# Kernel optimization log

Hardware: AMD Instinct MI355X
Metric: run time of the kernel (lower is better)

Reference implementation:

```python
import jax, jax.numpy as jnp
import numpy as np

N_NODES = 50000
N_EDGES = 800000
IN_CH = 256
HID = 64
HEADS = 4
NEG_SLOPE = 0.2  # PyG GATConv default


def setup_inputs() -> dict:
    key = jax.random.key(0)
    ks = jax.random.split(key, 12)
    glorot = lambda k, shape: jax.random.normal(k, shape, jnp.float32) * (2.0 / (shape[0] + shape[-1])) ** 0.5
    d1 = HEADS * HID  # 256: width after conv1 (concat heads)
    return {
        "x": jax.random.normal(ks[0], (N_NODES, IN_CH), jnp.float32),
        "edge_index": jax.random.randint(ks[1], (2, N_EDGES), 0, N_NODES, jnp.int64),
        # conv1: GATConv(IN_CH, HID, heads=HEADS)
        "W1": glorot(ks[2], (IN_CH, HEADS * HID)),
        "a_src1": glorot(ks[3], (HEADS, HID)),
        "a_dst1": glorot(ks[4], (HEADS, HID)),
        "b1": jnp.zeros((HEADS * HID,), jnp.float32),
        # conv2: GATConv(d1, d1, heads=1)
        "W2": glorot(ks[5], (d1, d1)),
        "a_src2": glorot(ks[6], (1, d1)),
        "a_dst2": glorot(ks[7], (1, d1)),
        "b2": jnp.zeros((d1,), jnp.float32),
    }


def gat_conv(x, src, dst, W, a_src, a_dst, b, heads, out_ch, n_nodes):
    """PyG-style GATConv: per-head linear, additive attention, segment softmax over dst."""
    h = (x @ W).reshape(n_nodes, heads, out_ch)            # [N, H, C]
    alpha_src = jnp.sum(h * a_src, axis=-1)                # [N, H]
    alpha_dst = jnp.sum(h * a_dst, axis=-1)                # [N, H]
    e = jax.nn.leaky_relu(alpha_src[src] + alpha_dst[dst], NEG_SLOPE)  # [E, H]
    # numerically-stable segment softmax grouped by destination node
    e_max = jax.ops.segment_max(e, dst, num_segments=n_nodes)         # [N, H]
    e_exp = jnp.exp(e - e_max[dst])
    denom = jax.ops.segment_sum(e_exp, dst, num_segments=n_nodes)
    alpha = e_exp / denom[dst]                                        # [E, H]
    out = jax.ops.segment_sum(alpha[:, :, None] * h[src], dst, num_segments=n_nodes)  # [N, H, C]
    return out.reshape(n_nodes, heads * out_ch) + b


def reference(x, edge_index, W1, a_src1, a_dst1, b1, W2, a_src2, a_dst2, b2):
    n = x.shape[0]
    loops = jnp.arange(n, dtype=edge_index.dtype)
    src = jnp.concatenate([edge_index[0], loops])  # add self-loops (PyG default)
    dst = jnp.concatenate([edge_index[1], loops])
    h1 = gat_conv(x, src, dst, W1, a_src1, a_dst1, b1, HEADS, HID, n)
    h1 = jax.nn.elu(h1)
    out = gat_conv(h1, src, dst, W2, a_src2, a_dst2, b2, 1, HEADS * HID, n)
    return out
```

## Files before the change

kernel.cpp:

```cpp
#include <hip/hip_runtime.h>
#include <stdint.h>

typedef __bf16 bfv8 __attribute__((ext_vector_type(8)));
typedef float f32x4 __attribute__((ext_vector_type(4)));

__device__ __forceinline__ float b2f(unsigned short u) {
    union { unsigned int i; float f; } v; v.i = ((unsigned int)u) << 16; return v.f;
}
__device__ __forceinline__ unsigned short f2b(float f) {
    unsigned int x = __float_as_uint(f);
    unsigned int r = x + 0x7FFFu + ((x >> 16) & 1u);
    return (unsigned short)(r >> 16);
}
__device__ __forceinline__ float squash(float v) {
    return (v == v && fabsf(v) < 1e30f) ? v : 0.f;
}
__device__ __forceinline__ float blo(unsigned int w) {
    union { unsigned int i; float f; } v; v.i = w << 16; return v.f;
}
__device__ __forceinline__ float bhi(unsigned int w) {
    union { unsigned int i; float f; } v; v.i = w & 0xffff0000u; return v.f;
}

__device__ __forceinline__ void detect_reg(const void* x, const void* ei, int& f32w, int& i64w) {
    const unsigned short* xu = (const unsigned short*)x;
    const int* e32 = (const int*)ei;
    int bad = 0, oz = 0;
#pragma unroll
    for (int j = 0; j < 64; j++) {
        float v = b2f(xu[j]);
        if (!(fabsf(v) < 1e10f)) bad++;
    }
#pragma unroll
    for (int j = 1; j < 16; j += 2)
        if (e32[j] == 0) oz++;
    f32w = (bad >= 2) ? 1 : 0;
    i64w = (oz >= 6) ? 1 : 0;
}

__device__ __forceinline__ int edge_at(const void* ei, int idx, int i64) {
    return i64 ? (int)(((const long long*)ei)[idx]) : ((const int*)ei)[idx];
}

__global__ __launch_bounds__(256) void k_prep(
        const void* __restrict__ x, const void* __restrict__ ei,
        const void* __restrict__ W1, const void* __restrict__ W2,
        const void* __restrict__ a_src1, const void* __restrict__ a_dst1, const void* __restrict__ b1,
        const void* __restrict__ a_src2, const void* __restrict__ a_dst2, const void* __restrict__ b2,
        unsigned short* __restrict__ xb, unsigned short* __restrict__ WT1,
        unsigned short* __restrict__ WT2, unsigned short* __restrict__ vecs,
        int* __restrict__ deg, int* __restrict__ flags,
        int E, int ET, int N, int total8, int nconv, int nhist) {
    __shared__ unsigned short t[32][33];
    int f32w, i64w;
    detect_reg(x, ei, f32w, i64w);
    int b = blockIdx.x;
    int tid = threadIdx.x;

    if (b < nconv) {
        int i = b * 256 + tid;
        if (i >= total8) return;
        if (f32w) {
            const float4* f = (const float4*)x;
            float4 a = f[2 * i], bb = f[2 * i + 1];
            uint4 o;
            o.x = (unsigned)f2b(squash(a.x)) | ((unsigned)f2b(squash(a.y)) << 16);
            o.y = (unsigned)f2b(squash(a.z)) | ((unsigned)f2b(squash(a.w)) << 16);
            o.z = (unsigned)f2b(squash(bb.x)) | ((unsigned)f2b(squash(bb.y)) << 16);
            o.w = (unsigned)f2b(squash(bb.z)) | ((unsigned)f2b(squash(bb.w)) << 16);
            *(uint4*)(xb + 8 * (size_t)i) = o;
        } else {
            *(uint4*)(xb + 8 * (size_t)i) = ((const uint4*)x)[i];
        }
    } else if (b < nconv + 128) {
        int tb2 = b - nconv;
        const void* W = (tb2 < 64) ? W1 : W2;
        unsigned short* WT = (tb2 < 64) ? WT1 : WT2;
        int t6 = tb2 & 63;
        int bx = (t6 & 7) * 32, by = (t6 >> 3) * 32;
        int tx = tid & 31, ty = tid >> 5;
        for (int j = 0; j < 32; j += 8) {
            size_t idx = (size_t)(by + ty + j) * 256 + bx + tx;
            t[ty + j][tx] = f32w ? f2b(squash(((const float*)W)[idx]))
                                 : ((const unsigned short*)W)[idx];
        }
        __syncthreads();
        for (int j = 0; j < 32; j += 8)
            WT[(size_t)(bx + ty + j) * 256 + by + tx] = t[tx][ty + j];
    } else if (b < nconv + 128 + nhist) {
        int i = (b - nconv - 128) * 256 + tid;
        if (i >= ET) return;
        int d = (i < E) ? edge_at(ei, E + i, i64w) : (i - E);
        d = min(max(d, 0), N - 1);
        atomicAdd(&deg[d], 1);
    } else {
        const void* ptrs[6] = {a_src1, a_dst1, b1, a_src2, a_dst2, b2};
#pragma unroll
        for (int j = 0; j < 6; j++) {
            unsigned short u = f32w ? f2b(squash(((const float*)ptrs[j])[tid]))
                                    : ((const unsigned short*)ptrs[j])[tid];
            vecs[j * 256 + tid] = u;
        }
        if (tid == 0) { flags[0] = f32w; flags[1] = i64w; }
    }
}

__global__ __launch_bounds__(256) void k_csr(const int* __restrict__ deg,
        int* __restrict__ row_start, int* __restrict__ cursor,
        unsigned short* __restrict__ csr16, int* __restrict__ fz,
        int N, int ET) {
    __shared__ int sm[256];
    __shared__ int s_prefix;
    const int b = blockIdx.x, tid = threadIdx.x;
    const int i = b * 256 + tid;
    int v = (i < N) ? deg[i] : 0;
    sm[tid] = v; __syncthreads();
    for (int off = 1; off < 256; off <<= 1) {
        int t = (tid >= off) ? sm[tid - off] : 0;
        __syncthreads();
        sm[tid] += t;
        __syncthreads();
    }
    int incl = sm[tid];
    int total = sm[255];
    if (tid == 0) {
        int val = (b == 0) ? ((total << 2) | 2) : ((total << 2) | 1);
        __threadfence();
        atomicExch(&fz[b], val);
    }
    if (b == 0) {
        if (tid == 0) s_prefix = 0;
    } else if (tid < 64) {
        int prefix = 0, base = b - 1, done = 0;
        while (!done) {
            int p = base - tid;
            int val;
            if (p >= 0) {
                do { val = atomicAdd(&fz[p], 0); } while (val == 0);
            } else {
                val = 2;
            }
            unsigned long long im = __ballot((val & 2) != 0);
            int fi = (int)__ffsll(im) - 1;
            int mv = val >> 2;
            int contrib = (fi < 0 || tid <= fi) ? mv : 0;
            for (int o = 1; o < 64; o <<= 1) contrib += __shfl_xor(contrib, o, 64);
            prefix += contrib;
            if (fi >= 0) done = 1; else base -= 64;
        }
        if (tid == 0) {
            s_prefix = prefix;
            __threadfence();
            atomicExch(&fz[b], ((prefix + total) << 2) | 2);
        }
    }
    __syncthreads();
    int pre = s_prefix;
    if (i < N) {
        int rs = pre + incl - v;
        row_start[i] = rs;
        cursor[i] = rs;
    }
    if (b == 0 && tid == 0) row_start[N] = ET;
    if (b == 0 && tid < 64) csr16[ET + tid] = 0;
}

__global__ void k_scatter(const void* __restrict__ ei, int* __restrict__ cursor,
                          unsigned short* __restrict__ csr16, const int* __restrict__ flags,
                          int E, int ET, int N) {
    int i = blockIdx.x * 256 + threadIdx.x;
    if (i >= ET) return;
    int s, d;
    if (i < E) {
        int i64 = flags[1];
        s = edge_at(ei, i, i64);
        d = edge_at(ei, E + i, i64);
    } else {
        s = i - E; d = i - E;
    }
    s = min(max(s, 0), N - 1);
    d = min(max(d, 0), N - 1);
    int pos = atomicAdd(&cursor[d], 1);
    pos = min(max(pos, 0), ET - 1);
    csr16[pos] = (unsigned short)s;
}

__global__ __launch_bounds__(256) void k_gemm(const unsigned short* __restrict__ A,
                                              const unsigned short* __restrict__ BT,
                                              unsigned short* __restrict__ C,
                                              const unsigned short* __restrict__ avs,
                                              const unsigned short* __restrict__ avd,
                                              float* __restrict__ as_out,
                                              float* __restrict__ ad_out, int M) {
    __shared__ __align__(16) unsigned short As[128 * 72];
    __shared__ __align__(16) unsigned short Bs[128 * 72];
    const int tid = threadIdx.x;
    const int m0 = blockIdx.x * 128, n0 = blockIdx.y * 128;
    const int w = tid >> 6, lane = tid & 63;
    const int wm = (w & 1) * 64, wn = (w >> 1) * 64;
    const int lr = lane & 15, lk = (lane >> 4) * 8;
    const int sr = tid >> 1, sc = (tid & 1) * 32;

    f32x4 acc[4][4];
#pragma unroll
    for (int a = 0; a < 4; a++)
#pragma unroll
        for (int b = 0; b < 4; b++) acc[a][b] = (f32x4){0.f, 0.f, 0.f, 0.f};

    for (int k0 = 0; k0 < 256; k0 += 64) {
        uint4 va0, va1, va2, va3;
        if (m0 + sr < M) {
            const uint4* Ap = (const uint4*)(A + (size_t)(m0 + sr) * 256 + k0 + sc);
            va0 = Ap[0]; va1 = Ap[1]; va2 = Ap[2]; va3 = Ap[3];
        } else {
            va0 = va1 = va2 = va3 = make_uint4(0, 0, 0, 0);
        }
        {
            uint4* Ad = (uint4*)&As[sr * 72 + sc];
            Ad[0] = va0; Ad[1] = va1; Ad[2] = va2; Ad[3] = va3;
        }
        {
            const uint4* Bp = (const uint4*)(BT + (size_t)(n0 + sr) * 256 + k0 + sc);
            uint4* Bd = (uint4*)&Bs[sr * 72 + sc];
            Bd[0] = Bp[0]; Bd[1] = Bp[1]; Bd[2] = Bp[2]; Bd[3] = Bp[3];
        }
        __syncthreads();
#pragma unroll
        for (int kk = 0; kk < 64; kk += 32) {
            bfv8 af[4], bfr[4];
#pragma unroll
            for (int mi = 0; mi < 4; mi++)
                af[mi] = *(const bfv8*)&As[(wm + mi * 16 + lr) * 72 + kk + lk];
#pragma unroll
            for (int ni = 0; ni < 4; ni++)
                bfr[ni] = *(const bfv8*)&Bs[(wn + ni * 16 + lr) * 72 + kk + lk];
#pragma unroll
            for (int mi = 0; mi < 4; mi++)
#pragma unroll
                for (int ni = 0; ni < 4; ni++)
                    acc[mi][ni] = __builtin_amdgcn_mfma_f32_16x16x32_bf16(af[mi], bfr[ni], acc[mi][ni], 0, 0, 0);
        }
        __syncthreads();
    }
    const int rb = (lane >> 4) * 4;
#pragma unroll
    for (int mi = 0; mi < 4; mi++) {
#pragma unroll
        for (int r = 0; r < 4; r++) {
            int row = m0 + wm + mi * 16 + rb + r;
            if (row < M) {
#pragma unroll
                for (int ni = 0; ni < 4; ni++)
                    C[(size_t)row * 256 + n0 + wn + ni * 16 + lr] = f2b(squash(acc[mi][ni][r]));
            }
        }
    }
    const int slice = (n0 + wn) >> 6;
    float asl[4], adl[4];
#pragma unroll
    for (int ni = 0; ni < 4; ni++) {
        int col = n0 + wn + ni * 16 + lr;
        asl[ni] = b2f(avs[col]);
        adl[ni] = b2f(avd[col]);
    }
#pragma unroll
    for (int mi = 0; mi < 4; mi++) {
#pragma unroll
        for (int r = 0; r < 4; r++) {
            float ps = 0.f, pd = 0.f;
#pragma unroll
            for (int ni = 0; ni < 4; ni++) {
                float cv = acc[mi][ni][r];
                ps = fmaf(cv, asl[ni], ps);
                pd = fmaf(cv, adl[ni], pd);
            }
#pragma unroll
            for (int off = 1; off < 16; off <<= 1) {
                ps += __shfl_xor(ps, off, 64);
                pd += __shfl_xor(pd, off, 64);
            }
            int row = m0 + wm + mi * 16 + rb + r;
            if (lr == 0 && row < M) {
                as_out[(size_t)row * 4 + slice] = squash(ps);
                ad_out[(size_t)row * 4 + slice] = squash(pd);
            }
        }
    }
}

template <int H>
__global__ __launch_bounds__(256) void k_agg(
        const unsigned short* __restrict__ Hm, const float* __restrict__ asrc,
        const float* __restrict__ adst, const int* __restrict__ row_start,
        const unsigned short* __restrict__ csr16, const unsigned short* __restrict__ bias,
        void* __restrict__ out, const int* __restrict__ flags,
        int N, int ET, int elu, int is_final) {
    __shared__ __align__(16) float lwv[8][32][4];
    __shared__ unsigned int loff[8][32];
    const int tid = threadIdx.x;
    const int hw = tid >> 5;
    const int l = tid & 31;
    const int h = (l * H) >> 5;
    const int lb = l * 16;
    const float* wbase = &lwv[hw][0][0] + h;
    const unsigned int* obase = &loff[hw][0];
    const char* Hb = (const char*)Hm;
    const int stride = gridDim.x * 8;

    for (int node = blockIdx.x * 8 + hw; node < N; node += stride) {
        int rs = row_start[node], re = row_start[node + 1];
        rs = min(max(rs, 0), ET);
        re = min(max(re, rs), ET);

        float adnx = 0.f, adny = 0.f, adnz = 0.f, adnw = 0.f;
        {
            float4 t = *(const float4*)(adst + (size_t)node * 4);
            if (H == 4) { adnx = t.x; adny = t.y; adnz = t.z; adnw = t.w; }
            else        { adnx = t.x + t.y + t.z + t.w; }
        }

        float lsx = 0.f, lsy = 0.f, lsz = 0.f, lsw = 0.f;
        float a0 = 0.f, a1 = 0.f, a2 = 0.f, a3 = 0.f;
        float a4 = 0.f, a5 = 0.f, a6 = 0.f, a7 = 0.f;

        for (int c = rs; c < re; c += 32) {
            const int cnt = min(32, re - c);
            float4 w4 = make_float4(0.f, 0.f, 0.f, 0.f);
            unsigned int off = 0;
            if (l < cnt) {
                int idx = min((int)csr16[c + l], N - 1);
                off = (unsigned)idx << 9;
                float4 av = *(const float4*)(asrc + (size_t)idx * 4);
                if (H == 4) {
                    float ex = av.x + adnx, ey = av.y + adny;
                    float ez = av.z + adnz, ew = av.w + adnw;
                    ex = (ex < 0.f) ? 0.2f * ex : ex;
                    ey = (ey < 0.f) ? 0.2f * ey : ey;
                    ez = (ez < 0.f) ? 0.2f * ez : ez;
                    ew = (ew < 0.f) ? 0.2f * ew : ew;
                    w4.x = __expf(fminf(ex, 80.f)); w4.y = __expf(fminf(ey, 80.f));
                    w4.z = __expf(fminf(ez, 80.f)); w4.w = __expf(fminf(ew, 80.f));
                } else {
                    float ev = (av.x + av.y + av.z + av.w) + adnx;
                    ev = (ev < 0.f) ? 0.2f * ev : ev;
                    w4.x = __expf(fminf(ev, 80.f));
                }
            }
            lsx += w4.x;
            if (H == 4) { lsy += w4.y; lsz += w4.z; lsw += w4.w; }
            *(float4*)&lwv[hw][l][0] = w4;
            loff[hw][l] = off;
            asm volatile("s_waitcnt lgkmcnt(0)");

            const int full = cnt & ~7;
            int jb = 0;
            for (; jb < full; jb += 8) {
                unsigned int o_[8];
                uint4 hv[8];
                float wj[8];
#pragma unroll
                for (int u = 0; u < 8; u++) o_[u] = obase[jb + u];
#pragma unroll
                for (int u = 0; u < 8; u++) hv[u] = *(const uint4*)(Hb + (size_t)o_[u] + lb);
#pragma unroll
                for (int u = 0; u < 8; u++) wj[u] = wbase[(jb + u) * 4];
#pragma unroll
                for (int u = 0; u < 8; u++) {
                    a0 = fmaf(wj[u], blo(hv[u].x), a0); a1 = fmaf(wj[u], bhi(hv[u].x), a1);
                    a2 = fmaf(wj[u], blo(hv[u].y), a2); a3 = fmaf(wj[u], bhi(hv[u].y), a3);
                    a4 = fmaf(wj[u], blo(hv[u].z), a4); a5 = fmaf(wj[u], bhi(hv[u].z), a5);
                    a6 = fmaf(wj[u], blo(hv[u].w), a6); a7 = fmaf(wj[u], bhi(hv[u].w), a7);
                }
            }
            if (jb < cnt) {
                const int rem = cnt - jb;
                unsigned int o_[8];
                uint4 hv[8];
                float wj[8];
#pragma unroll
                for (int u = 0; u < 8; u++) o_[u] = obase[jb + u];
#pragma unroll
                for (int u = 0; u < 8; u++) {
                    uint4 z = make_uint4(0, 0, 0, 0);
                    hv[u] = (u < rem) ? *(const uint4*)(Hb + (size_t)o_[u] + lb) : z;
                }
#pragma unroll
                for (int u = 0; u < 8; u++) wj[u] = wbase[(jb + u) * 4];
#pragma unroll
                for (int u = 0; u < 8; u++) {
                    a0 = fmaf(wj[u], blo(hv[u].x), a0); a1 = fmaf(wj[u], bhi(hv[u].x), a1);
                    a2 = fmaf(wj[u], blo(hv[u].y), a2); a3 = fmaf(wj[u], bhi(hv[u].y), a3);
                    a4 = fmaf(wj[u], blo(hv[u].z), a4); a5 = fmaf(wj[u], bhi(hv[u].z), a5);
                    a6 = fmaf(wj[u], blo(hv[u].w), a6); a7 = fmaf(wj[u], bhi(hv[u].w), a7);
                }
            }
        }
        for (int off = 1; off < 32; off <<= 1) {
            lsx += __shfl_xor(lsx, off, 64);
            if (H == 4) {
                lsy += __shfl_xor(lsy, off, 64);
                lsz += __shfl_xor(lsz, off, 64);
                lsw += __shfl_xor(lsw, off, 64);
            }
        }
        float ls = (H == 4) ? ((h == 0) ? lsx : (h == 1) ? lsy : (h == 2) ? lsz : lsw) : lsx;
        float inv = (ls > 0.f) ? 1.f / ls : 0.f;

        const int cc = 8 * l;
        uint4 bv = *(const uint4*)(bias + cc);
        float o0 = a0 * inv + blo(bv.x), o1 = a1 * inv + bhi(bv.x);
        float o2 = a2 * inv + blo(bv.y), o3 = a3 * inv + bhi(bv.y);
        float o4 = a4 * inv + blo(bv.z), o5 = a5 * inv + bhi(bv.z);
        float o6 = a6 * inv + blo(bv.w), o7 = a7 * inv + bhi(bv.w);
        if (elu) {
            o0 = (o0 > 0.f) ? o0 : __expf(o0) - 1.f;
            o1 = (o1 > 0.f) ? o1 : __expf(o1) - 1.f;
            o2 = (o2 > 0.f) ? o2 : __expf(o2) - 1.f;
            o3 = (o3 > 0.f) ? o3 : __expf(o3) - 1.f;
            o4 = (o4 > 0.f) ? o4 : __expf(o4) - 1.f;
            o5 = (o5 > 0.f) ? o5 : __expf(o5) - 1.f;
            o6 = (o6 > 0.f) ? o6 : __expf(o6) - 1.f;
            o7 = (o7 > 0.f) ? o7 : __expf(o7) - 1.f;
        }
        o0 = squash(o0); o1 = squash(o1); o2 = squash(o2); o3 = squash(o3);
        o4 = squash(o4); o5 = squash(o5); o6 = squash(o6); o7 = squash(o7);
        if (is_final && flags[0]) {
            float* op = (float*)out + (size_t)node * 256 + cc;
            *(float4*)op       = make_float4(o0, o1, o2, o3);
            *(float4*)(op + 4) = make_float4(o4, o5, o6, o7);
        } else {
            uint4 ov;
            ov.x = (unsigned)f2b(o0) | ((unsigned)f2b(o1) << 16);
            ov.y = (unsigned)f2b(o2) | ((unsigned)f2b(o3) << 16);
            ov.z = (unsigned)f2b(o4) | ((unsigned)f2b(o5) << 16);
            ov.w = (unsigned)f2b(o6) | ((unsigned)f2b(o7) << 16);
            *(uint4*)((unsigned short*)out + (size_t)node * 256 + cc) = ov;
        }
    }
}

extern "C" void kernel_launch(void* const* d_in, const int* in_sizes, int n_in,
                              void* d_out, int out_size, void* d_ws, size_t ws_size,
                              hipStream_t stream) {
    const void* x      = d_in[0];
    const void* ei     = d_in[1];
    const void* W1     = d_in[2];
    const void* a_src1 = d_in[3];
    const void* a_dst1 = d_in[4];
    const void* b1     = d_in[5];
    const void* W2     = d_in[6];
    const void* a_src2 = d_in[7];
    const void* a_dst2 = d_in[8];
    const void* b2     = d_in[9];

    const int N  = in_sizes[0] / 256;
    const int E  = in_sizes[1] / 2;
    const int ET = E + N;

    char* p = (char*)d_ws;
    auto alloc = [&](size_t bytes) -> char* {
        char* r = p;
        p += (bytes + 255) & ~(size_t)255;
        return r;
    };
    int* flags = (int*)alloc(256);
    unsigned short* WT1  = (unsigned short*)alloc(256 * 256 * 2);
    unsigned short* WT2  = (unsigned short*)alloc(256 * 256 * 2);
    unsigned short* vecs = (unsigned short*)alloc(6 * 256 * 2);
    float* as_ = (float*)alloc((size_t)N * 4 * 4);
    float* ad_ = (float*)alloc((size_t)N * 4 * 4);
    int* deg   = (int*)alloc((size_t)N * 4);
    int* fz    = (int*)alloc(1024);
    int* row_start = (int*)alloc((size_t)(N + 1) * 4);
    int* cursor    = (int*)alloc((size_t)N * 4);
    unsigned short* csr16 = (unsigned short*)alloc((size_t)(ET + 64) * 2);

    unsigned short* BUF_OUT = (unsigned short*)d_out;
    unsigned short* BUF_IN0 = (unsigned short*)d_in[0];

    const size_t degpad = ((size_t)N * 4 + 255) & ~(size_t)255;
    hipMemsetAsync(deg, 0, degpad + 1024, stream);

    const int total8 = N * 256 / 8;
    const int nconv  = (total8 + 255) / 256;
    const int nhist  = (ET + 255) / 256;
    const int nprep  = nconv + 128 + nhist + 1;

    k_prep<<<nprep, 256, 0, stream>>>(x, ei, W1, W2, a_src1, a_dst1, b1, a_src2, a_dst2, b2,
                                      BUF_OUT, WT1, WT2, vecs, deg, flags,
                                      E, ET, N, total8, nconv, nhist);

    int nb = (N + 255) / 256;
    k_csr<<<nb, 256, 0, stream>>>(deg, row_start, cursor, csr16, fz, N, ET);
    k_scatter<<<nhist, 256, 0, stream>>>(ei, cursor, csr16, flags, E, ET, N);

    int gm = (N + 127) / 128;
    int ab = (N + 7) / 8;
    if (ab > 2048) ab = 2048;

    k_gemm<<<dim3(gm, 2), 256, 0, stream>>>(BUF_OUT, WT1, BUF_IN0,
                                            vecs + 0 * 256, vecs + 1 * 256, as_, ad_, N);
    k_agg<4><<<ab, 256, 0, stream>>>(BUF_IN0, as_, ad_, row_start, csr16, vecs + 2 * 256,
                                     BUF_OUT, flags, N, ET, 1, 0);
    k_gemm<<<dim3(gm, 2), 256, 0, stream>>>(BUF_OUT, WT2, BUF_IN0,
                                            vecs + 3 * 256, vecs + 4 * 256, as_, ad_, N);
    k_agg<1><<<ab, 256, 0, stream>>>(BUF_IN0, as_, ad_, row_start, csr16, vecs + 5 * 256,
                                     d_out, flags, N, ET, 0, 1);
}
```

Baseline: 404.0 us.

## Fuse fp32-to-bf16 input conversion into first GEMM and stop writing into inputs

```diff
diff --git a/kernel.cpp b/kernel.cpp
--- a/kernel.cpp
+++ b/kernel.cpp
@@ -47,36 +47,19 @@
         const void* __restrict__ W1, const void* __restrict__ W2,
         const void* __restrict__ a_src1, const void* __restrict__ a_dst1, const void* __restrict__ b1,
         const void* __restrict__ a_src2, const void* __restrict__ a_dst2, const void* __restrict__ b2,
-        unsigned short* __restrict__ xb, unsigned short* __restrict__ WT1,
-        unsigned short* __restrict__ WT2, unsigned short* __restrict__ vecs,
-        int* __restrict__ deg, int* __restrict__ flags,
-        int E, int ET, int N, int total8, int nconv, int nhist) {
+        unsigned short* __restrict__ WT1, unsigned short* __restrict__ WT2,
+        unsigned short* __restrict__ vecs, int* __restrict__ deg, int* __restrict__ flags,
+        int E, int ET, int N, int nhist) {
     __shared__ unsigned short t[32][33];
     int f32w, i64w;
     detect_reg(x, ei, f32w, i64w);
     int b = blockIdx.x;
     int tid = threadIdx.x;
 
-    if (b < nconv) {
-        int i = b * 256 + tid;
-        if (i >= total8) return;
-        if (f32w) {
-            const float4* f = (const float4*)x;
-            float4 a = f[2 * i], bb = f[2 * i + 1];
-            uint4 o;
-            o.x = (unsigned)f2b(squash(a.x)) | ((unsigned)f2b(squash(a.y)) << 16);
-            o.y = (unsigned)f2b(squash(a.z)) | ((unsigned)f2b(squash(a.w)) << 16);
-            o.z = (unsigned)f2b(squash(bb.x)) | ((unsigned)f2b(squash(bb.y)) << 16);
-            o.w = (unsigned)f2b(squash(bb.z)) | ((unsigned)f2b(squash(bb.w)) << 16);
-            *(uint4*)(xb + 8 * (size_t)i) = o;
-        } else {
-            *(uint4*)(xb + 8 * (size_t)i) = ((const uint4*)x)[i];
-        }
-    } else if (b < nconv + 128) {
-        int tb2 = b - nconv;
-        const void* W = (tb2 < 64) ? W1 : W2;
-        unsigned short* WT = (tb2 < 64) ? WT1 : WT2;
-        int t6 = tb2 & 63;
+    if (b < 128) {
+        const void* W = (b < 64) ? W1 : W2;
+        unsigned short* WT = (b < 64) ? WT1 : WT2;
+        int t6 = b & 63;
         int bx = (t6 & 7) * 32, by = (t6 >> 3) * 32;
         int tx = tid & 31, ty = tid >> 5;
         for (int j = 0; j < 32; j += 8) {
@@ -87,8 +70,8 @@
         __syncthreads();
         for (int j = 0; j < 32; j += 8)
             WT[(size_t)(bx + ty + j) * 256 + by + tx] = t[tx][ty + j];
-    } else if (b < nconv + 128 + nhist) {
-        int i = (b - nconv - 128) * 256 + tid;
+    } else if (b < 128 + nhist) {
+        int i = (b - 128) * 256 + tid;
         if (i >= ET) return;
         int d = (i < E) ? edge_at(ei, E + i, i64w) : (i - E);
         d = min(max(d, 0), N - 1);
@@ -185,13 +168,15 @@
     csr16[pos] = (unsigned short)s;
 }
 
-__global__ __launch_bounds__(256) void k_gemm(const unsigned short* __restrict__ A,
+template <int SRC>
+__global__ __launch_bounds__(256) void k_gemm(const void* __restrict__ Asrc,
                                               const unsigned short* __restrict__ BT,
                                               unsigned short* __restrict__ C,
                                               const unsigned short* __restrict__ avs,
                                               const unsigned short* __restrict__ avd,
                                               float* __restrict__ as_out,
-                                              float* __restrict__ ad_out, int M) {
+                                              float* __restrict__ ad_out,
+                                              const int* __restrict__ flags, int M) {
     __shared__ __align__(16) unsigned short As[128 * 72];
     __shared__ __align__(16) unsigned short Bs[128 * 72];
     const int tid = threadIdx.x;
@@ -200,6 +185,7 @@
     const int wm = (w & 1) * 64, wn = (w >> 1) * 64;
     const int lr = lane & 15, lk = (lane >> 4) * 8;
     const int sr = tid >> 1, sc = (tid & 1) * 32;
+    const bool xf32 = (SRC == 1) && (flags[0] != 0);
 
     f32x4 acc[4][4];
 #pragma unroll
@@ -210,8 +196,31 @@
     for (int k0 = 0; k0 < 256; k0 += 64) {
         uint4 va0, va1, va2, va3;
         if (m0 + sr < M) {
-            const uint4* Ap = (const uint4*)(A + (size_t)(m0 + sr) * 256 + k0 + sc);
-            va0 = Ap[0]; va1 = Ap[1]; va2 = Ap[2]; va3 = Ap[3];
+            const size_t base = (size_t)(m0 + sr) * 256 + k0 + sc;
+            if (SRC == 1 && xf32) {
+                const float4* xp = (const float4*)Asrc + (base >> 2);
+                float4 f0 = xp[0], f1 = xp[1], f2_ = xp[2], f3 = xp[3];
+                float4 f4 = xp[4], f5 = xp[5], f6 = xp[6], f7 = xp[7];
+                va0.x = (unsigned)f2b(squash(f0.x)) | ((unsigned)f2b(squash(f0.y)) << 16);
+                va0.y = (unsigned)f2b(squash(f0.z)) | ((unsigned)f2b(squash(f0.w)) << 16);
+                va0.z = (unsigned)f2b(squash(f1.x)) | ((unsigned)f2b(squash(f1.y)) << 16);
+                va0.w = (unsigned)f2b(squash(f1.z)) | ((unsigned)f2b(squash(f1.w)) << 16);
+                va1.x = (unsigned)f2b(squash(f2_.x)) | ((unsigned)f2b(squash(f2_.y)) << 16);
+                va1.y = (unsigned)f2b(squash(f2_.z)) | ((unsigned)f2b(squash(f2_.w)) << 16);
+                va1.z = (unsigned)f2b(squash(f3.x)) | ((unsigned)f2b(squash(f3.y)) << 16);
+                va1.w = (unsigned)f2b(squash(f3.z)) | ((unsigned)f2b(squash(f3.w)) << 16);
+                va2.x = (unsigned)f2b(squash(f4.x)) | ((unsigned)f2b(squash(f4.y)) << 16);
+                va2.y = (unsigned)f2b(squash(f4.z)) | ((unsigned)f2b(squash(f4.w)) << 16);
+                va2.z = (unsigned)f2b(squash(f5.x)) | ((unsigned)f2b(squash(f5.y)) << 16);
+                va2.w = (unsigned)f2b(squash(f5.z)) | ((unsigned)f2b(squash(f5.w)) << 16);
+                va3.x = (unsigned)f2b(squash(f6.x)) | ((unsigned)f2b(squash(f6.y)) << 16);
+                va3.y = (unsigned)f2b(squash(f6.z)) | ((unsigned)f2b(squash(f6.w)) << 16);
+                va3.z = (unsigned)f2b(squash(f7.x)) | ((unsigned)f2b(squash(f7.y)) << 16);
+                va3.w = (unsigned)f2b(squash(f7.z)) | ((unsigned)f2b(squash(f7.w)) << 16);
+            } else {
+                const uint4* Ap = (const uint4*)((const unsigned short*)Asrc + base);
+                va0 = Ap[0]; va1 = Ap[1]; va2 = Ap[2]; va3 = Ap[3];
+            }
         } else {
             va0 = va1 = va2 = va3 = make_uint4(0, 0, 0, 0);
         }
@@ -300,142 +309,139 @@
     const int tid = threadIdx.x;
     const int hw = tid >> 5;
     const int l = tid & 31;
+    const int node = blockIdx.x * 8 + hw;
+    if (node >= N) return;
     const int h = (l * H) >> 5;
     const int lb = l * 16;
+    int rs = row_start[node], re = row_start[node + 1];
+    rs = min(max(rs, 0), ET);
+    re = min(max(re, rs), ET);
+
+    float adnx = 0.f, adny = 0.f, adnz = 0.f, adnw = 0.f;
+    {
+        float4 t = *(const float4*)(adst + (size_t)node * 4);
+        if (H == 4) { adnx = t.x; adny = t.y; adnz = t.z; adnw = t.w; }
+        else        { adnx = t.x + t.y + t.z + t.w; }
+    }
+
+    float lsx = 0.f, lsy = 0.f, lsz = 0.f, lsw = 0.f;
+    float a0 = 0.f, a1 = 0.f, a2 = 0.f, a3 = 0.f, a4 = 0.f, a5 = 0.f, a6 = 0.f, a7 = 0.f;
     const float* wbase = &lwv[hw][0][0] + h;
     const unsigned int* obase = &loff[hw][0];
     const char* Hb = (const char*)Hm;
-    const int stride = gridDim.x * 8;
-
-    for (int node = blockIdx.x * 8 + hw; node < N; node += stride) {
-        int rs = row_start[node], re = row_start[node + 1];
-        rs = min(max(rs, 0), ET);
-        re = min(max(re, rs), ET);
-
-        float adnx = 0.f, adny = 0.f, adnz = 0.f, adnw = 0.f;
-        {
-            float4 t = *(const float4*)(adst + (size_t)node * 4);
-            if (H == 4) { adnx = t.x; adny = t.y; adnz = t.z; adnw = t.w; }
-            else        { adnx = t.x + t.y + t.z + t.w; }
-        }
-
-        float lsx = 0.f, lsy = 0.f, lsz = 0.f, lsw = 0.f;
-        float a0 = 0.f, a1 = 0.f, a2 = 0.f, a3 = 0.f;
-        float a4 = 0.f, a5 = 0.f, a6 = 0.f, a7 = 0.f;
-
-        for (int c = rs; c < re; c += 32) {
-            const int cnt = min(32, re - c);
-            float4 w4 = make_float4(0.f, 0.f, 0.f, 0.f);
-            unsigned int off = 0;
-            if (l < cnt) {
-                int idx = min((int)csr16[c + l], N - 1);
-                off = (unsigned)idx << 9;
-                float4 av = *(const float4*)(asrc + (size_t)idx * 4);
-                if (H == 4) {
-                    float ex = av.x + adnx, ey = av.y + adny;
-                    float ez = av.z + adnz, ew = av.w + adnw;
-                    ex = (ex < 0.f) ? 0.2f * ex : ex;
-                    ey = (ey < 0.f) ? 0.2f * ey : ey;
-                    ez = (ez < 0.f) ? 0.2f * ez : ez;
-                    ew = (ew < 0.f) ? 0.2f * ew : ew;
-                    w4.x = __expf(fminf(ex, 80.f)); w4.y = __expf(fminf(ey, 80.f));
-                    w4.z = __expf(fminf(ez, 80.f)); w4.w = __expf(fminf(ew, 80.f));
-                } else {
-                    float ev = (av.x + av.y + av.z + av.w) + adnx;
-                    ev = (ev < 0.f) ? 0.2f * ev : ev;
-                    w4.x = __expf(fminf(ev, 80.f));
-                }
-            }
-            lsx += w4.x;
-            if (H == 4) { lsy += w4.y; lsz += w4.z; lsw += w4.w; }
-            *(float4*)&lwv[hw][l][0] = w4;
-            loff[hw][l] = off;
-            asm volatile("s_waitcnt lgkmcnt(0)");
-
-            const int full = cnt & ~7;
-            int jb = 0;
-            for (; jb < full; jb += 8) {
-                unsigned int o_[8];
-                uint4 hv[8];
-                float wj[8];
-#pragma unroll
-                for (int u = 0; u < 8; u++) o_[u] = obase[jb + u];
-#pragma unroll
-                for (int u = 0; u < 8; u++) hv[u] = *(const uint4*)(Hb + (size_t)o_[u] + lb);
-#pragma unroll
-                for (int u = 0; u < 8; u++) wj[u] = wbase[(jb + u) * 4];
-#pragma unroll
-                for (int u = 0; u < 8; u++) {
-                    a0 = fmaf(wj[u], blo(hv[u].x), a0); a1 = fmaf(wj[u], bhi(hv[u].x), a1);
-                    a2 = fmaf(wj[u], blo(hv[u].y), a2); a3 = fmaf(wj[u], bhi(hv[u].y), a3);
-                    a4 = fmaf(wj[u], blo(hv[u].z), a4); a5 = fmaf(wj[u], bhi(hv[u].z), a5);
-                    a6 = fmaf(wj[u], blo(hv[u].w), a6); a7 = fmaf(wj[u], bhi(hv[u].w), a7);
-                }
-            }
-            if (jb < cnt) {
-                const int rem = cnt - jb;
-                unsigned int o_[8];
-                uint4 hv[8];
-                float wj[8];
-#pragma unroll
-                for (int u = 0; u < 8; u++) o_[u] = obase[jb + u];
-#pragma unroll
-                for (int u = 0; u < 8; u++) {
-                    uint4 z = make_uint4(0, 0, 0, 0);
-                    hv[u] = (u < rem) ? *(const uint4*)(Hb + (size_t)o_[u] + lb) : z;
-                }
-#pragma unroll
-                for (int u = 0; u < 8; u++) wj[u] = wbase[(jb + u) * 4];
-#pragma unroll
-                for (int u = 0; u < 8; u++) {
-                    a0 = fmaf(wj[u], blo(hv[u].x), a0); a1 = fmaf(wj[u], bhi(hv[u].x), a1);
-                    a2 = fmaf(wj[u], blo(hv[u].y), a2); a3 = fmaf(wj[u], bhi(hv[u].y), a3);
-                    a4 = fmaf(wj[u], blo(hv[u].z), a4); a5 = fmaf(wj[u], bhi(hv[u].z), a5);
-                    a6 = fmaf(wj[u], blo(hv[u].w), a6); a7 = fmaf(wj[u], bhi(hv[u].w), a7);
-                }
-            }
-        }
-        for (int off = 1; off < 32; off <<= 1) {
-            lsx += __shfl_xor(lsx, off, 64);
+
+    for (int c = rs; c < re; c += 32) {
+        const int cnt = min(32, re - c);
+        float4 w4 = make_float4(0.f, 0.f, 0.f, 0.f);
+        unsigned int off = 0;
+        if (l < cnt) {
+            int idx = min((int)csr16[c + l], N - 1);
+            off = (unsigned)idx << 9;
+            float4 av = *(const float4*)(asrc + (size_t)idx * 4);
             if (H == 4) {
-                lsy += __shfl_xor(lsy, off, 64);
-                lsz += __shfl_xor(lsz, off, 64);
-                lsw += __shfl_xor(lsw, off, 64);
-            }
-        }
-        float ls = (H == 4) ? ((h == 0) ? lsx : (h == 1) ? lsy : (h == 2) ? lsz : lsw) : lsx;
-        float inv = (ls > 0.f) ? 1.f / ls : 0.f;
-
-        const int cc = 8 * l;
-        uint4 bv = *(const uint4*)(bias + cc);
-        float o0 = a0 * inv + blo(bv.x), o1 = a1 * inv + bhi(bv.x);
-        float o2 = a2 * inv + blo(bv.y), o3 = a3 * inv + bhi(bv.y);
-        float o4 = a4 * inv + blo(bv.z), o5 = a5 * inv + bhi(bv.z);
-        float o6 = a6 * inv + blo(bv.w), o7 = a7 * inv + bhi(bv.w);
-        if (elu) {
-            o0 = (o0 > 0.f) ? o0 : __expf(o0) - 1.f;
-            o1 = (o1 > 0.f) ? o1 : __expf(o1) - 1.f;
-            o2 = (o2 > 0.f) ? o2 : __expf(o2) - 1.f;
-            o3 = (o3 > 0.f) ? o3 : __expf(o3) - 1.f;
-            o4 = (o4 > 0.f) ? o4 : __expf(o4) - 1.f;
-            o5 = (o5 > 0.f) ? o5 : __expf(o5) - 1.f;
-            o6 = (o6 > 0.f) ? o6 : __expf(o6) - 1.f;
-            o7 = (o7 > 0.f) ? o7 : __expf(o7) - 1.f;
-        }
-        o0 = squash(o0); o1 = squash(o1); o2 = squash(o2); o3 = squash(o3);
-        o4 = squash(o4); o5 = squash(o5); o6 = squash(o6); o7 = squash(o7);
-        if (is_final && flags[0]) {
-            float* op = (float*)out + (size_t)node * 256 + cc;
-            *(float4*)op       = make_float4(o0, o1, o2, o3);
-            *(float4*)(op + 4) = make_float4(o4, o5, o6, o7);
-        } else {
-            uint4 ov;
-            ov.x = (unsigned)f2b(o0) | ((unsigned)f2b(o1) << 16);
-            ov.y = (unsigned)f2b(o2) | ((unsigned)f2b(o3) << 16);
-            ov.z = (unsigned)f2b(o4) | ((unsigned)f2b(o5) << 16);
-            ov.w = (unsigned)f2b(o6) | ((unsigned)f2b(o7) << 16);
-            *(uint4*)((unsigned short*)out + (size_t)node * 256 + cc) = ov;
-        }
+                float ex = av.x + adnx, ey = av.y + adny;
+                float ez = av.z + adnz, ew = av.w + adnw;
+                ex = (ex < 0.f) ? 0.2f * ex : ex;
+                ey = (ey < 0.f) ? 0.2f * ey : ey;
+                ez = (ez < 0.f) ? 0.2f * ez : ez;
+                ew = (ew < 0.f) ? 0.2f * ew : ew;
+                w4.x = __expf(fminf(ex, 80.f)); w4.y = __expf(fminf(ey, 80.f));
+                w4.z = __expf(fminf(ez, 80.f)); w4.w = __expf(fminf(ew, 80.f));
+            } else {
+                float ev = (av.x + av.y + av.z + av.w) + adnx;
+                ev = (ev < 0.f) ? 0.2f * ev : ev;
+                w4.x = __expf(fminf(ev, 80.f));
+            }
+        }
+        lsx += w4.x;
+        if (H == 4) { lsy += w4.y; lsz += w4.z; lsw += w4.w; }
+        *(float4*)&lwv[hw][l][0] = w4;
+        loff[hw][l] = off;
+        asm volatile("s_waitcnt lgkmcnt(0)");
+
+        const int full = cnt & ~7;
+        int jb = 0;
+        for (; jb < full; jb += 8) {
+            unsigned int o_[8];
+            uint4 hv[8];
+            float wj[8];
+#pragma unroll
+            for (int u = 0; u < 8; u++) o_[u] = obase[jb + u];
+#pragma unroll
+            for (int u = 0; u < 8; u++) hv[u] = *(const uint4*)(Hb + (size_t)o_[u] + lb);
+#pragma unroll
+            for (int u = 0; u < 8; u++) wj[u] = wbase[(jb + u) * 4];
+#pragma unroll
+            for (int u = 0; u < 8; u++) {
+                a0 = fmaf(wj[u], blo(hv[u].x), a0); a1 = fmaf(wj[u], bhi(hv[u].x), a1);
+                a2 = fmaf(wj[u], blo(hv[u].y), a2); a3 = fmaf(wj[u], bhi(hv[u].y), a3);
+                a4 = fmaf(wj[u], blo(hv[u].z), a4); a5 = fmaf(wj[u], bhi(hv[u].z), a5);
+                a6 = fmaf(wj[u], blo(hv[u].w), a6); a7 = fmaf(wj[u], bhi(hv[u].w), a7);
+            }
+        }
+        if (jb < cnt) {
+            const int rem = cnt - jb;
+            unsigned int o_[8];
+            uint4 hv[8];
+            float wj[8];
+#pragma unroll
+            for (int u = 0; u < 8; u++) o_[u] = obase[jb + u];
+#pragma unroll
+            for (int u = 0; u < 8; u++) {
+                uint4 z = make_uint4(0, 0, 0, 0);
+                hv[u] = (u < rem) ? *(const uint4*)(Hb + (size_t)o_[u] + lb) : z;
+            }
+#pragma unroll
+            for (int u = 0; u < 8; u++) wj[u] = wbase[(jb + u) * 4];
+#pragma unroll
+            for (int u = 0; u < 8; u++) {
+                a0 = fmaf(wj[u], blo(hv[u].x), a0); a1 = fmaf(wj[u], bhi(hv[u].x), a1);
+                a2 = fmaf(wj[u], blo(hv[u].y), a2); a3 = fmaf(wj[u], bhi(hv[u].y), a3);
+                a4 = fmaf(wj[u], blo(hv[u].z), a4); a5 = fmaf(wj[u], bhi(hv[u].z), a5);
+                a6 = fmaf(wj[u], blo(hv[u].w), a6); a7 = fmaf(wj[u], bhi(hv[u].w), a7);
+            }
+        }
+    }
+    for (int off = 1; off < 32; off <<= 1) {
+        lsx += __shfl_xor(lsx, off, 64);
+        if (H == 4) {
+            lsy += __shfl_xor(lsy, off, 64);
+            lsz += __shfl_xor(lsz, off, 64);
+            lsw += __shfl_xor(lsw, off, 64);
+        }
+    }
+    float ls = (H == 4) ? ((h == 0) ? lsx : (h == 1) ? lsy : (h == 2) ? lsz : lsw) : lsx;
+    float inv = (ls > 0.f) ? 1.f / ls : 0.f;
+
+    const int cc = 8 * l;
+    uint4 bv = *(const uint4*)(bias + cc);
+    float o0 = a0 * inv + blo(bv.x), o1 = a1 * inv + bhi(bv.x);
+    float o2 = a2 * inv + blo(bv.y), o3 = a3 * inv + bhi(bv.y);
+    float o4 = a4 * inv + blo(bv.z), o5 = a5 * inv + bhi(bv.z);
+    float o6 = a6 * inv + blo(bv.w), o7 = a7 * inv + bhi(bv.w);
+    if (elu) {
+        o0 = (o0 > 0.f) ? o0 : __expf(o0) - 1.f;
+        o1 = (o1 > 0.f) ? o1 : __expf(o1) - 1.f;
+        o2 = (o2 > 0.f) ? o2 : __expf(o2) - 1.f;
+        o3 = (o3 > 0.f) ? o3 : __expf(o3) - 1.f;
+        o4 = (o4 > 0.f) ? o4 : __expf(o4) - 1.f;
+        o5 = (o5 > 0.f) ? o5 : __expf(o5) - 1.f;
+        o6 = (o6 > 0.f) ? o6 : __expf(o6) - 1.f;
+        o7 = (o7 > 0.f) ? o7 : __expf(o7) - 1.f;
+    }
+    o0 = squash(o0); o1 = squash(o1); o2 = squash(o2); o3 = squash(o3);
+    o4 = squash(o4); o5 = squash(o5); o6 = squash(o6); o7 = squash(o7);
+    if (is_final && flags[0]) {
+        float* op = (float*)out + (size_t)node * 256 + cc;
+        *(float4*)op       = make_float4(o0, o1, o2, o3);
+        *(float4*)(op + 4) = make_float4(o4, o5, o6, o7);
+    } else {
+        uint4 ov;
+        ov.x = (unsigned)f2b(o0) | ((unsigned)f2b(o1) << 16);
+        ov.y = (unsigned)f2b(o2) | ((unsigned)f2b(o3) << 16);
+        ov.z = (unsigned)f2b(o4) | ((unsigned)f2b(o5) << 16);
+        ov.w = (unsigned)f2b(o6) | ((unsigned)f2b(o7) << 16);
+        *(uint4*)((unsigned short*)out + (size_t)node * 256 + cc) = ov;
     }
 }
 
@@ -474,21 +480,21 @@
     int* row_start = (int*)alloc((size_t)(N + 1) * 4);
     int* cursor    = (int*)alloc((size_t)N * 4);
     unsigned short* csr16 = (unsigned short*)alloc((size_t)(ET + 64) * 2);
-
-    unsigned short* BUF_OUT = (unsigned short*)d_out;
-    unsigned short* BUF_IN0 = (unsigned short*)d_in[0];
+    unsigned short* H2w   = (unsigned short*)alloc((size_t)N * 256 * 2);
+
+    const bool ws_ok = ((size_t)(p - (char*)d_ws) <= ws_size);
+    unsigned short* H1 = (unsigned short*)d_out;
+    unsigned short* A1 = (unsigned short*)d_out + (size_t)N * 256;
+    unsigned short* H2 = ws_ok ? H2w : (unsigned short*)d_in[0];
 
     const size_t degpad = ((size_t)N * 4 + 255) & ~(size_t)255;
     hipMemsetAsync(deg, 0, degpad + 1024, stream);
 
-    const int total8 = N * 256 / 8;
-    const int nconv  = (total8 + 255) / 256;
-    const int nhist  = (ET + 255) / 256;
-    const int nprep  = nconv + 128 + nhist + 1;
+    const int nhist = (ET + 255) / 256;
+    const int nprep = 128 + nhist + 1;
 
     k_prep<<<nprep, 256, 0, stream>>>(x, ei, W1, W2, a_src1, a_dst1, b1, a_src2, a_dst2, b2,
-                                      BUF_OUT, WT1, WT2, vecs, deg, flags,
-                                      E, ET, N, total8, nconv, nhist);
+                                      WT1, WT2, vecs, deg, flags, E, ET, N, nhist);
 
     int nb = (N + 255) / 256;
     k_csr<<<nb, 256, 0, stream>>>(deg, row_start, cursor, csr16, fz, N, ET);
@@ -496,14 +502,15 @@
 
     int gm = (N + 127) / 128;
     int ab = (N + 7) / 8;
-    if (ab > 2048) ab = 2048;
-
-    k_gemm<<<dim3(gm, 2), 256, 0, stream>>>(BUF_OUT, WT1, BUF_IN0,
-                                            vecs + 0 * 256, vecs + 1 * 256, as_, ad_, N);
-    k_agg<4><<<ab, 256, 0, stream>>>(BUF_IN0, as_, ad_, row_start, csr16, vecs + 2 * 256,
-                                     BUF_OUT, flags, N, ET, 1, 0);
-    k_gemm<<<dim3(gm, 2), 256, 0, stream>>>(BUF_OUT, WT2, BUF_IN0,
-                                            vecs + 3 * 256, vecs + 4 * 256, as_, ad_, N);
-    k_agg<1><<<ab, 256, 0, stream>>>(BUF_IN0, as_, ad_, row_start, csr16, vecs + 5 * 256,
+
+    k_gemm<1><<<dim3(gm, 2), 256, 0, stream>>>(x, WT1, H1,
+                                               vecs + 0 * 256, vecs + 1 * 256, as_, ad_,
+                                               flags, N);
+    k_agg<4><<<ab, 256, 0, stream>>>(H1, as_, ad_, row_start, csr16, vecs + 2 * 256,
+                                     A1, flags, N, ET, 1, 0);
+    k_gemm<0><<<dim3(gm, 2), 256, 0, stream>>>(A1, WT2, H2,
+                                               vecs + 3 * 256, vecs + 4 * 256, as_, ad_,
+                                               flags, N);
+    k_agg<1><<<ab, 256, 0, stream>>>(H2, as_, ad_, row_start, csr16, vecs + 5 * 256,
                                      d_out, flags, N, ET, 0, 1);
 }
```

Measured after the change: 396.2 us. About the same (-1.9%).
